# Optimization experiments

Hardware: AMD Instinct MI355X
Metric: run time of the kernel (lower is better)

## Reference

```python
import jax, jax.numpy as jnp
import numpy as np

N_NODES = 100_000
N_EDGES = 1_600_000
N_GRAPHS = 64
N_OPS = 120
OP_EMB = 32
NODE_FEAT = 140
CFG_FEAT = 18
LIN_OUT = 128
H = 64
EPS = 1e-12  # F.normalize eps


def _glorot(k, shape):
    s = (6.0 / (shape[0] + shape[1])) ** 0.5
    return jax.random.uniform(k, shape, jnp.float32, -s, s)


def setup_inputs() -> dict:
    key = jax.random.key(0)
    ks = iter(jax.random.split(key, 40))
    inp = {
        "node_feat": jax.random.normal(next(ks), (N_NODES, NODE_FEAT), jnp.float32),
        "node_config_feat": jax.random.normal(next(ks), (N_NODES, CFG_FEAT), jnp.float32),
        "node_opcode": jax.random.randint(next(ks), (N_NODES,), 0, N_OPS, jnp.int32),
        "edge_index": jax.random.randint(next(ks), (2, N_EDGES), 0, N_NODES, jnp.int32),
        # contiguous graph assignment -> every one of the 64 graphs is non-empty
        "batch": ((jnp.arange(N_NODES) * N_GRAPHS) // N_NODES).astype(jnp.int32),
        "op_emb": jax.random.normal(next(ks), (N_OPS, OP_EMB), jnp.float32),
        "lin_w": _glorot(next(ks), (NODE_FEAT + OP_EMB + CFG_FEAT, LIN_OUT)),
        "lin_b": jnp.zeros((LIN_OUT,), jnp.float32),
        "post_w": _glorot(next(ks), (H, 1)),
        "post_b": jnp.zeros((1,), jnp.float32),
    }
    in_dims = [LIN_OUT, H, H]
    for l, d in enumerate(in_dims):
        inp[f"proj_w{l}"] = _glorot(next(ks), (d, d))
        inp[f"proj_b{l}"] = jnp.zeros((d,), jnp.float32)
        inp[f"wl{l}"] = _glorot(next(ks), (d, H))
        inp[f"bl{l}"] = jnp.zeros((H,), jnp.float32)
        inp[f"wr{l}"] = _glorot(next(ks), (d, H))
    return inp


def _sage_conv(x, src, dst, pw, pb, wl, bl, wr):
    # PyG SAGEConv(normalize=True, project=True): messages use projected x,
    # root term uses the un-projected x; mean aggregation over in-edges.
    xp = jax.nn.relu(x @ pw + pb)                                  # (N, d)
    msg = jax.ops.segment_sum(xp[src], dst, num_segments=N_NODES)  # (N, d)
    deg = jax.ops.segment_sum(jnp.ones((src.shape[0],), x.dtype), dst,
                              num_segments=N_NODES)
    mean = msg / jnp.maximum(deg, 1.0)[:, None]
    out = mean @ wl + bl + x @ wr                                   # (N, H)
    n = jnp.linalg.norm(out, axis=-1, keepdims=True)
    return out / jnp.maximum(n, EPS)


def reference(node_feat, node_config_feat, node_opcode, edge_index, batch,
              op_emb, lin_w, lin_b, post_w, post_b,
              proj_w0, proj_b0, wl0, bl0, wr0,
              proj_w1, proj_b1, wl1, bl1, wr1,
              proj_w2, proj_b2, wl2, bl2, wr2):
    x = jnp.concatenate([node_feat, op_emb[node_opcode], node_config_feat], axis=-1)
    x = jax.nn.relu(x @ lin_w + lin_b)  # (N, 128)
    src, dst = edge_index[0], edge_index[1]
    layers = [(proj_w0, proj_b0, wl0, bl0, wr0),
              (proj_w1, proj_b1, wl1, bl1, wr1),
              (proj_w2, proj_b2, wl2, bl2, wr2)]
    for pw, pb, wl, bl, wr in layers:
        x = _sage_conv(x, src, dst, pw, pb, wl, bl, wr)
    # global max pool + global mean pool per graph
    x_max = jax.ops.segment_max(x, batch, num_segments=N_GRAPHS)
    cnt = jax.ops.segment_sum(jnp.ones((x.shape[0],), x.dtype), batch,
                              num_segments=N_GRAPHS)
    x_mean = jax.ops.segment_sum(x, batch, num_segments=N_GRAPHS) / cnt[:, None]
    x_graph = x_max + x_mean
    x_graph = x_graph / jnp.linalg.norm(x_graph, axis=-1, keepdims=True)
    return x_graph @ post_w + post_b  # (B, 1)
```

## Files before the change

### kernel.cpp

```cpp
#include <hip/hip_runtime.h>
#include <hip/hip_bf16.h>
#include <math.h>

#define N_NODES   100000
#define N_EDGES   1600000
#define N_GRAPHS  64
#define NF_D      140
#define OP_EMB_D  32
#define CFG_D     18
#define K_EMB     192
#define NB_SCAN   391

typedef __attribute__((ext_vector_type(8))) short short8;
typedef __attribute__((ext_vector_type(4))) float f32x4;

__device__ __forceinline__ unsigned fenc(float f) {
    unsigned u = __float_as_uint(f);
    return (u & 0x80000000u) ? ~u : (u | 0x80000000u);
}
__device__ __forceinline__ float fdec(unsigned u) {
    unsigned v = (u & 0x80000000u) ? (u & 0x7FFFFFFFu) : ~u;
    return __uint_as_float(v);
}
__device__ __forceinline__ unsigned short f2bf(float f) {
    unsigned u = __float_as_uint(f);
    return (unsigned short)((u + 0x7FFFu + ((u >> 16) & 1u)) >> 16);
}
__device__ __forceinline__ float bf2f(unsigned short h) {
    return __uint_as_float((unsigned)h << 16);
}
__device__ __forceinline__ short8 ld_frag(const unsigned short* p) {
    union { uint4 u; short8 s; } c;
    c.u = *(const uint4*)p;
    return c.s;
}


__global__ void hist_kernel(const int* __restrict__ dst, int* __restrict__ cnt) {
    int e = blockIdx.x * blockDim.x + threadIdx.x;
    if (e < N_EDGES) atomicAdd(&cnt[__builtin_nontemporal_load(dst + e)], 1);
}

__global__ __launch_bounds__(256) void blocksum_kernel(const int* __restrict__ cnt,
                                                       int* __restrict__ bsum) {
    const int tid = threadIdx.x, lane = tid & 63, wave = tid >> 6;
    int i = blockIdx.x * 256 + tid;
    int v = (i < N_NODES) ? cnt[i] : 0;
    #pragma unroll
    for (int off = 32; off > 0; off >>= 1) v += __shfl_xor(v, off, 64);
    __shared__ int wsum[4];
    if (lane == 0) wsum[wave] = v;
    __syncthreads();
    if (tid == 0) bsum[blockIdx.x] = wsum[0] + wsum[1] + wsum[2] + wsum[3];
}

__global__ __launch_bounds__(512) void scanbsum_kernel(int* __restrict__ bsum) {
    __shared__ int s[512];
    const int t = threadIdx.x;
    int v0 = (t < NB_SCAN) ? bsum[t] : 0;
    s[t] = v0;
    __syncthreads();
    for (int off = 1; off < 512; off <<= 1) {
        int add = (t >= off) ? s[t - off] : 0;
        __syncthreads();
        s[t] += add;
        __syncthreads();
    }
    if (t < NB_SCAN) bsum[t] = s[t] - v0;
}

__global__ __launch_bounds__(256) void offsets_kernel(int* __restrict__ cnt,
                                                      const int* __restrict__ bsum,
                                                      int* __restrict__ row_start) {
    const int t = threadIdx.x;
    const int i = blockIdx.x * 256 + t;
    int v0 = (i < N_NODES) ? cnt[i] : 0;
    __shared__ int s[256];
    s[t] = v0;
    __syncthreads();
    for (int off = 1; off < 256; off <<= 1) {
        int add = (t >= off) ? s[t - off] : 0;
        __syncthreads();
        s[t] += add;
        __syncthreads();
    }
    const int excl = s[t] - v0 + bsum[blockIdx.x];
    if (i < N_NODES) {
        row_start[i] = excl;
        cnt[i] = excl;
    }
    if (i == N_NODES - 1) row_start[N_NODES] = excl + v0;
}

__global__ void fill_kernel(const int* __restrict__ src, const int* __restrict__ dst,
                            int* __restrict__ cursor, int* __restrict__ nbr) {
    const int range = blockIdx.x & 7;
    const int lo = range * (N_NODES / 8);
    const int hi = lo + (N_NODES / 8);
    const int groups = gridDim.x >> 3;
    const int sub = blockIdx.x >> 3;
    for (int e = sub * blockDim.x + threadIdx.x; e < N_EDGES;
         e += groups * blockDim.x) {
        const int d = __builtin_nontemporal_load(dst + e);
        if (d >= lo && d < hi) {
            const int s = __builtin_nontemporal_load(src + e);
            const int slot = atomicAdd(&cursor[d], 1);
            nbr[slot] = s;
        }
    }
}


__global__ __launch_bounds__(256) void concat_kernel(
    const float* __restrict__ node_feat, const float* __restrict__ cfg,
    const int* __restrict__ opcode, const float* __restrict__ op_emb,
    unsigned short* __restrict__ x0)
{
    const long long total = (long long)N_NODES * 96;
    for (long long idx = (long long)blockIdx.x * blockDim.x + threadIdx.x;
         idx < total; idx += (long long)gridDim.x * blockDim.x) {
        const int n  = (int)(idx / 96);
        const int c  = 2 * (int)(idx % 96);
        float2 v;
        if (c < NF_D) {
            v = *(const float2*)(node_feat + (long long)n * NF_D + c);
        } else if (c < NF_D + OP_EMB_D) {
            const int op = opcode[n];
            v = *(const float2*)(op_emb + op * OP_EMB_D + (c - NF_D));
        } else if (c < 190) {
            v = *(const float2*)(cfg + (long long)n * CFG_D + (c - NF_D - OP_EMB_D));
        } else {
            v.x = 0.f; v.y = 0.f;
        }
        const unsigned pk = ((unsigned)f2bf(v.y) << 16) | (unsigned)f2bf(v.x);
        *(unsigned*)(x0 + (long long)n * K_EMB + c) = pk;
    }
}

struct WDesc { const float* src; unsigned short* dst; int K, Ksrc, M, off; };
struct WPack { WDesc d[10]; int total; };

__global__ __launch_bounds__(256) void pack_w_kernel(WPack p) {
    const int idx = blockIdx.x * blockDim.x + threadIdx.x;
    if (idx >= p.total) return;
    #pragma unroll
    for (int i = 0; i < 10; ++i) {
        const WDesc d = p.d[i];
        if (idx >= d.off && idx < d.off + d.K * d.M) {
            const int r    = idx - d.off;
            const int kc   = r / (d.M * 32);
            const int rem  = r % (d.M * 32);
            const int mt   = rem / 512;
            const int rem2 = rem % 512;
            const int lane = rem2 >> 3;
            const int j    = rem2 & 7;
            const int k = kc * 32 + (lane >> 4) * 8 + j;
            const int m = mt * 16 + (lane & 15);
            const float v = (k < d.Ksrc) ? d.src[(long long)k * d.M + m] : 0.f;
            d.dst[r] = f2bf(v);
            return;
        }
    }
}

template <int M, int K, bool BIAS, bool RELU, bool OBF16>
__global__ __launch_bounds__(256) void mfma_gemm(
    const unsigned short* __restrict__ x,
    const unsigned short* __restrict__ wpk, const float* __restrict__ b,
    void* __restrict__ outv, int N)
{
    constexpr int MT = M / 16;
    constexpr int KC = K / 32;
    const int tid = threadIdx.x, wave = tid >> 6, lane = tid & 63;
    const int wid = blockIdx.x * 4 + wave;
    if (wid >= (N >> 5)) return;
    const int nb   = wid << 5;
    const int l15  = lane & 15;
    const int quad = lane >> 4;

    f32x4 acc[2][MT];
    #pragma unroll
    for (int mt = 0; mt < MT; ++mt) {
        #pragma unroll
        for (int r = 0; r < 4; ++r) {
            const float bv = BIAS ? b[mt * 16 + quad * 4 + r] : 0.f;
            acc[0][mt][r] = bv;
            acc[1][mt][r] = bv;
        }
    }
    #pragma unroll
    for (int kc = 0; kc < KC; ++kc) {
        const short8 b0 = ld_frag(x + (long long)(nb + l15)      * K + kc * 32 + quad * 8);
        const short8 b1 = ld_frag(x + (long long)(nb + 16 + l15) * K + kc * 32 + quad * 8);
        #pragma unroll
        for (int mt = 0; mt < MT; ++mt) {
            const short8 a = ld_frag(wpk + ((long long)(kc * MT + mt) * 64 + lane) * 8);
            acc[0][mt] = __builtin_amdgcn_mfma_f32_16x16x32_bf16(a, b0, acc[0][mt], 0, 0, 0);
            acc[1][mt] = __builtin_amdgcn_mfma_f32_16x16x32_bf16(a, b1, acc[1][mt], 0, 0, 0);
        }
    }
    #pragma unroll
    for (int s = 0; s < 2; ++s) {
        const long long row = nb + s * 16 + l15;
        if (OBF16) {
            unsigned short* orow = (unsigned short*)outv + row * M;
            #pragma unroll
            for (int mt = 0; mt < MT; ++mt) {
                float f0 = acc[s][mt][0], f1 = acc[s][mt][1];
                float f2 = acc[s][mt][2], f3 = acc[s][mt][3];
                if (RELU) {
                    f0 = fmaxf(f0, 0.f); f1 = fmaxf(f1, 0.f);
                    f2 = fmaxf(f2, 0.f); f3 = fmaxf(f3, 0.f);
                }
                uint2 pk;
                pk.x = ((unsigned)f2bf(f1) << 16) | (unsigned)f2bf(f0);
                pk.y = ((unsigned)f2bf(f3) << 16) | (unsigned)f2bf(f2);
                *(uint2*)(orow + mt * 16 + quad * 4) = pk;
            }
        } else {
            float* orow = (float*)outv + row * M;
            #pragma unroll
            for (int mt = 0; mt < MT; ++mt) {
                f32x4 v = acc[s][mt];
                if (RELU) {
                    v[0] = fmaxf(v[0], 0.f); v[1] = fmaxf(v[1], 0.f);
                    v[2] = fmaxf(v[2], 0.f); v[3] = fmaxf(v[3], 0.f);
                }
                *(f32x4*)(orow + mt * 16 + quad * 4) = v;
            }
        }
    }
}

template <bool OBF16>
__global__ __launch_bounds__(256, 8) void combine_kernel(
    const int* __restrict__ row_start, const int* __restrict__ nbr,
    const unsigned short* __restrict__ yp, const float* __restrict__ r,
    void* __restrict__ out)
{
    const int tid = threadIdx.x, wave = tid >> 6, lane = tid & 63;
    for (int n = blockIdx.x * 4 + wave; n < N_NODES; n += gridDim.x * 4) {
        const int rs = row_start[n], re = row_start[n + 1];
        float macc[8];
        #pragma unroll
        for (int q = 0; q < 8; ++q) macc[q] = 0.f;
        for (int eb = rs; eb < re; eb += 64) {
            const int cnt = min(64, re - eb);
            const int my = (eb + lane < re) ? nbr[eb + lane] : 0;
            for (int j2 = 0; j2 < cnt; j2 += 8) {
                #pragma unroll
                for (int q = 0; q < 8; ++q) {
                    const int jj = j2 + q;
                    const int s = __shfl(my, (jj < cnt) ? jj : 0, 64);
                    const float v = bf2f(yp[(long long)s * 64 + lane]);
                    if (jj < cnt) macc[q] += v;
                }
            }
        }
        const float m = ((macc[0] + macc[1]) + (macc[2] + macc[3]))
                      + ((macc[4] + macc[5]) + (macc[6] + macc[7]));
        float acc = r[(long long)n * 64 + lane] + m / fmaxf((float)(re - rs), 1.0f);
        float sq = acc * acc;
        #pragma unroll
        for (int off = 32; off > 0; off >>= 1) sq += __shfl_xor(sq, off, 64);
        const float res = acc / fmaxf(sqrtf(sq), 1e-12f);
        if (OBF16)
            ((unsigned short*)out)[(long long)n * 64 + lane] = f2bf(res);
        else
            ((float*)out)[(long long)n * 64 + lane] = res;
    }
}


__global__ __launch_bounds__(256) void pool_kernel(
    const float* __restrict__ x, const int* __restrict__ batch,
    float* __restrict__ gsum, unsigned* __restrict__ gmax, float* __restrict__ gcnt)
{
    __shared__ float    lsum[2][64];
    __shared__ unsigned lmax[2][64];
    __shared__ int      lcnt[2];
    const int tid = threadIdx.x, wave = tid >> 6, lane = tid & 63;
    if (tid < 128) { lsum[tid >> 6][tid & 63] = 0.f; lmax[tid >> 6][tid & 63] = 0u; }
    if (tid < 2) lcnt[tid] = 0;
    __syncthreads();
    const int base = blockIdx.x * 256;
    const int g0 = batch[base];
    float a0 = 0.f, a1 = 0.f, x0 = -INFINITY, x1 = -INFINITY;
    int c0 = 0, c1 = 0;
    for (int nn = 0; nn < 64; ++nn) {
        const int n = base + wave * 64 + nn;
        if (n >= N_NODES) break;
        const float v = x[(long long)n * 64 + lane];
        const int slot = batch[n] - g0;
        if (slot == 0)      { a0 += v; x0 = fmaxf(x0, v); c0++; }
        else if (slot == 1) { a1 += v; x1 = fmaxf(x1, v); c1++; }
        else {
            const int g = g0 + slot;
            atomicAdd(&gsum[g * 64 + lane], v);
            atomicMax(&gmax[g * 64 + lane], fenc(v));
            if (lane == 0) atomicAdd(&gcnt[g], 1.f);
        }
    }
    if (c0) { atomicAdd(&lsum[0][lane], a0); atomicMax(&lmax[0][lane], fenc(x0));
              if (lane == 0) atomicAdd(&lcnt[0], c0); }
    if (c1) { atomicAdd(&lsum[1][lane], a1); atomicMax(&lmax[1][lane], fenc(x1));
              if (lane == 0) atomicAdd(&lcnt[1], c1); }
    __syncthreads();
    if (tid < 128) {
        const int slot = tid >> 6, k = tid & 63;
        if (lcnt[slot] > 0) {
            const int g = g0 + slot;
            atomicAdd(&gsum[g * 64 + k], lsum[slot][k]);
            atomicMax(&gmax[g * 64 + k], lmax[slot][k]);
            if (k == 0) atomicAdd(&gcnt[g], (float)lcnt[slot]);
        }
    }
}

__global__ void finalize_kernel(const float* __restrict__ gsum, const unsigned* __restrict__ gmax,
                                const float* __restrict__ gcnt, const float* __restrict__ post_w,
                                const float* __restrict__ post_b, float* __restrict__ out)
{
    const int g = blockIdx.x;
    const int k = threadIdx.x;
    const float cnt = gcnt[g];
    const float v = fdec(gmax[g * 64 + k]) + gsum[g * 64 + k] / cnt;
    const float w = post_w[k];
    float sq = v * v, dw = v * w;
    #pragma unroll
    for (int off = 32; off > 0; off >>= 1) {
        sq += __shfl_xor(sq, off, 64);
        dw += __shfl_xor(dw, off, 64);
    }
    if (k == 0) out[g] = dw / sqrtf(sq) + post_b[0];
}

extern "C" void kernel_launch(void* const* d_in, const int* in_sizes, int n_in,
                              void* d_out, int out_size, void* d_ws, size_t ws_size,
                              hipStream_t stream)
{
    const float* node_feat = (const float*)d_in[0];
    const float* cfg       = (const float*)d_in[1];
    const int*   opcode    = (const int*)  d_in[2];
    const int*   edge      = (const int*)  d_in[3];
    const int*   batch     = (const int*)  d_in[4];
    const float* op_emb    = (const float*)d_in[5];
    const float* lin_w     = (const float*)d_in[6];
    const float* lin_b     = (const float*)d_in[7];
    const float* post_w    = (const float*)d_in[8];
    const float* post_b    = (const float*)d_in[9];
    const float* pw[3] = {(const float*)d_in[10], (const float*)d_in[15], (const float*)d_in[20]};
    const float* pb[3] = {(const float*)d_in[11], (const float*)d_in[16], (const float*)d_in[21]};
    const float* wl[3] = {(const float*)d_in[12], (const float*)d_in[17], (const float*)d_in[22]};
    const float* bl[3] = {(const float*)d_in[13], (const float*)d_in[18], (const float*)d_in[23]};
    const float* wr[3] = {(const float*)d_in[14], (const float*)d_in[19], (const float*)d_in[24]};
    const int* srcp = edge;
    const int* dstp = edge + N_EDGES;

    float* ws   = (float*)d_ws;
    int*   nbr       = (int*)(ws + 32000000);
    int*   row_start = (int*)(ws + 33600000);
    int*   cnt       = (int*)(ws + 33700064);
    int*   bsum      = (int*)(ws + 33800064);
    float* gsum      = ws + 33825152;
    float* gcnt      = ws + 33829248;
    unsigned* gmax   = (unsigned*)(ws + 33829312);
    unsigned short* wpk_base = (unsigned short*)(ws + 34000000);

    const int OFF_EMB = 0;
    const int OFF_PW0 = 24576;
    const int OFF_WL0 = 24576 + 16384;
    const int OFF_WR0 = OFF_WL0 + 8192;
    const int OFF_PW1 = OFF_WR0 + 8192;
    const int OFF_WL1 = OFF_PW1 + 4096;
    const int OFF_WR1 = OFF_WL1 + 4096;
    const int OFF_PW2 = OFF_WR1 + 4096;
    const int OFF_WL2 = OFF_PW2 + 4096;
    const int OFF_WR2 = OFF_WL2 + 4096;
    const int W_TOTAL = OFF_WR2 + 4096;

    unsigned short* A_bf    = (unsigned short*)ws;
    unsigned short* C2_bf   = (unsigned short*)ws;
    float*          C3      = ws;
    unsigned short* C1_bf   = (unsigned short*)(ws + 6400000);
    unsigned short* X0_bf   = (unsigned short*)(ws + 12800000);
    unsigned short* xp128_bf= (unsigned short*)(ws + 12800000);
    unsigned short* xp64_bf = (unsigned short*)(ws + 12800000);
    float*          r       = ws + 19200000;
    unsigned short* yp      = (unsigned short*)(ws + 25600000);

    hipMemsetAsync(cnt, 0, (size_t)N_NODES * 4, stream);
    hipMemsetAsync(gsum, 0, (size_t)(4096 + 64 + 4096) * 4, stream);

    WPack wp;
    wp.d[0] = { lin_w, wpk_base + OFF_EMB, K_EMB, 190, 128, OFF_EMB };
    wp.d[1] = { pw[0], wpk_base + OFF_PW0, 128, 128, 128, OFF_PW0 };
    wp.d[2] = { wl[0], wpk_base + OFF_WL0, 128, 128,  64, OFF_WL0 };
    wp.d[3] = { wr[0], wpk_base + OFF_WR0, 128, 128,  64, OFF_WR0 };
    wp.d[4] = { pw[1], wpk_base + OFF_PW1,  64,  64,  64, OFF_PW1 };
    wp.d[5] = { wl[1], wpk_base + OFF_WL1,  64,  64,  64, OFF_WL1 };
    wp.d[6] = { wr[1], wpk_base + OFF_WR1,  64,  64,  64, OFF_WR1 };
    wp.d[7] = { pw[2], wpk_base + OFF_PW2,  64,  64,  64, OFF_PW2 };
    wp.d[8] = { wl[2], wpk_base + OFF_WL2,  64,  64,  64, OFF_WL2 };
    wp.d[9] = { wr[2], wpk_base + OFF_WR2,  64,  64,  64, OFF_WR2 };
    wp.total = W_TOTAL;
    pack_w_kernel<<<(W_TOTAL + 255) / 256, 256, 0, stream>>>(wp);

    hist_kernel<<<(N_EDGES + 255) / 256, 256, 0, stream>>>(dstp, cnt);
    blocksum_kernel<<<NB_SCAN, 256, 0, stream>>>(cnt, bsum);
    scanbsum_kernel<<<1, 512, 0, stream>>>(bsum);
    offsets_kernel<<<NB_SCAN, 256, 0, stream>>>(cnt, bsum, row_start);
    fill_kernel<<<8 * 256, 256, 0, stream>>>(srcp, dstp, cnt, nbr);

    concat_kernel<<<4096, 256, 0, stream>>>(node_feat, cfg, opcode, op_emb, X0_bf);

    const int GW = (N_NODES / 32 + 3) / 4;

    mfma_gemm<128, 192, true, true, true><<<GW, 256, 0, stream>>>(
        X0_bf, wpk_base + OFF_EMB, lin_b, A_bf, N_NODES);

    mfma_gemm<128, 128, true,  true,  true ><<<GW, 256, 0, stream>>>(
        A_bf, wpk_base + OFF_PW0, pb[0], xp128_bf, N_NODES);
    mfma_gemm< 64, 128, false, false, true ><<<GW, 256, 0, stream>>>(
        xp128_bf, wpk_base + OFF_WL0, nullptr, yp, N_NODES);
    mfma_gemm< 64, 128, true,  false, false><<<GW, 256, 0, stream>>>(
        A_bf, wpk_base + OFF_WR0, bl[0], r, N_NODES);
    combine_kernel<true><<<2048, 256, 0, stream>>>(row_start, nbr, yp, r, C1_bf);

    mfma_gemm< 64, 64, true,  true,  true ><<<GW, 256, 0, stream>>>(
        C1_bf, wpk_base + OFF_PW1, pb[1], xp64_bf, N_NODES);
    mfma_gemm< 64, 64, false, false, true ><<<GW, 256, 0, stream>>>(
        xp64_bf, wpk_base + OFF_WL1, nullptr, yp, N_NODES);
    mfma_gemm< 64, 64, true,  false, false><<<GW, 256, 0, stream>>>(
        C1_bf, wpk_base + OFF_WR1, bl[1], r, N_NODES);
    combine_kernel<true><<<2048, 256, 0, stream>>>(row_start, nbr, yp, r, C2_bf);

    mfma_gemm< 64, 64, true,  true,  true ><<<GW, 256, 0, stream>>>(
        C2_bf, wpk_base + OFF_PW2, pb[2], xp64_bf, N_NODES);
    mfma_gemm< 64, 64, false, false, true ><<<GW, 256, 0, stream>>>(
        xp64_bf, wpk_base + OFF_WL2, nullptr, yp, N_NODES);
    mfma_gemm< 64, 64, true,  false, false><<<GW, 256, 0, stream>>>(
        C2_bf, wpk_base + OFF_WR2, bl[2], r, N_NODES);
    combine_kernel<false><<<2048, 256, 0, stream>>>(row_start, nbr, yp, r, C3);

    pool_kernel<<<NB_SCAN, 256, 0, stream>>>(C3, batch, gsum, gmax, gcnt);
    finalize_kernel<<<N_GRAPHS, 64, 0, stream>>>(gsum, gmax, gcnt, post_w, post_b,
                                                 (float*)d_out);
}
```

Baseline: 661.7 us.

## Fuse per-layer projection, neighbor and root GEMMs into one kernel

Each SAGE layer used three separate GEMM launches: projection with ReLU written to global memory, a second GEMM reading it back for the neighbor weights, and a root GEMM re-reading the input. A new fused kernel reads the input tile once, computes the projection and root outputs together, stages the ReLU'd bf16 projection in per-wave shared memory, and applies the neighbor weights from there. This removes the xp intermediate round trip through global memory and two launches per layer, at the cost of more accumulator registers and shared memory per block, which may lower occupancy.

```diff
diff --git a/kernel.cpp b/kernel.cpp
--- a/kernel.cpp
+++ b/kernel.cpp
@@ -232,6 +232,113 @@
     }
 }
 
+template <int D>
+__global__ __launch_bounds__(256) void fused_layer(
+    const unsigned short* __restrict__ x,
+    const unsigned short* __restrict__ wpw, const float* __restrict__ pb,
+    const unsigned short* __restrict__ wwl,
+    const unsigned short* __restrict__ wwr, const float* __restrict__ bl,
+    unsigned short* __restrict__ yp, float* __restrict__ rout, int N)
+{
+    constexpr int MT  = D / 16;
+    constexpr int KC  = D / 32;
+    constexpr int LST = D + 8;
+    __shared__ unsigned short xpl[4][32][LST];
+    const int tid = threadIdx.x, wave = tid >> 6, lane = tid & 63;
+    const int wid = blockIdx.x * 4 + wave;
+    if (wid >= (N >> 5)) return;
+    const int nb   = wid << 5;
+    const int l15  = lane & 15;
+    const int quad = lane >> 4;
+
+    f32x4 axp[2][MT];
+    f32x4 ar[2][4];
+    #pragma unroll
+    for (int mt = 0; mt < MT; ++mt) {
+        #pragma unroll
+        for (int q = 0; q < 4; ++q) {
+            const float bv = pb[mt * 16 + quad * 4 + q];
+            axp[0][mt][q] = bv;
+            axp[1][mt][q] = bv;
+        }
+    }
+    #pragma unroll
+    for (int mt = 0; mt < 4; ++mt) {
+        #pragma unroll
+        for (int q = 0; q < 4; ++q) {
+            const float bv = bl[mt * 16 + quad * 4 + q];
+            ar[0][mt][q] = bv;
+            ar[1][mt][q] = bv;
+        }
+    }
+    #pragma unroll
+    for (int kc = 0; kc < KC; ++kc) {
+        const short8 b0 = ld_frag(x + (long long)(nb + l15)      * D + kc * 32 + quad * 8);
+        const short8 b1 = ld_frag(x + (long long)(nb + 16 + l15) * D + kc * 32 + quad * 8);
+        #pragma unroll
+        for (int mt = 0; mt < MT; ++mt) {
+            const short8 a = ld_frag(wpw + ((long long)(kc * MT + mt) * 64 + lane) * 8);
+            axp[0][mt] = __builtin_amdgcn_mfma_f32_16x16x32_bf16(a, b0, axp[0][mt], 0, 0, 0);
+            axp[1][mt] = __builtin_amdgcn_mfma_f32_16x16x32_bf16(a, b1, axp[1][mt], 0, 0, 0);
+        }
+        #pragma unroll
+        for (int mt = 0; mt < 4; ++mt) {
+            const short8 a = ld_frag(wwr + ((long long)(kc * 4 + mt) * 64 + lane) * 8);
+            ar[0][mt] = __builtin_amdgcn_mfma_f32_16x16x32_bf16(a, b0, ar[0][mt], 0, 0, 0);
+            ar[1][mt] = __builtin_amdgcn_mfma_f32_16x16x32_bf16(a, b1, ar[1][mt], 0, 0, 0);
+        }
+    }
+    #pragma unroll
+    for (int s = 0; s < 2; ++s) {
+        float* orow = rout + (long long)(nb + s * 16 + l15) * 64;
+        #pragma unroll
+        for (int mt = 0; mt < 4; ++mt)
+            *(f32x4*)(orow + mt * 16 + quad * 4) = ar[s][mt];
+    }
+    #pragma unroll
+    for (int s = 0; s < 2; ++s) {
+        #pragma unroll
+        for (int mt = 0; mt < MT; ++mt) {
+            float f0 = fmaxf(axp[s][mt][0], 0.f), f1 = fmaxf(axp[s][mt][1], 0.f);
+            float f2 = fmaxf(axp[s][mt][2], 0.f), f3 = fmaxf(axp[s][mt][3], 0.f);
+            uint2 pk;
+            pk.x = ((unsigned)f2bf(f1) << 16) | (unsigned)f2bf(f0);
+            pk.y = ((unsigned)f2bf(f3) << 16) | (unsigned)f2bf(f2);
+            *(uint2*)&xpl[wave][s * 16 + l15][mt * 16 + quad * 4] = pk;
+        }
+    }
+    asm volatile("s_waitcnt lgkmcnt(0)" ::: "memory");
+
+    f32x4 ay[2][4];
+    #pragma unroll
+    for (int mt = 0; mt < 4; ++mt) {
+        #pragma unroll
+        for (int q = 0; q < 4; ++q) { ay[0][mt][q] = 0.f; ay[1][mt][q] = 0.f; }
+    }
+    #pragma unroll
+    for (int kc = 0; kc < KC; ++kc) {
+        const short8 b0 = ld_frag(&xpl[wave][l15]     [kc * 32 + quad * 8]);
+        const short8 b1 = ld_frag(&xpl[wave][16 + l15][kc * 32 + quad * 8]);
+        #pragma unroll
+        for (int mt = 0; mt < 4; ++mt) {
+            const short8 a = ld_frag(wwl + ((long long)(kc * 4 + mt) * 64 + lane) * 8);
+            ay[0][mt] = __builtin_amdgcn_mfma_f32_16x16x32_bf16(a, b0, ay[0][mt], 0, 0, 0);
+            ay[1][mt] = __builtin_amdgcn_mfma_f32_16x16x32_bf16(a, b1, ay[1][mt], 0, 0, 0);
+        }
+    }
+    #pragma unroll
+    for (int s = 0; s < 2; ++s) {
+        unsigned short* orow = yp + (long long)(nb + s * 16 + l15) * 64;
+        #pragma unroll
+        for (int mt = 0; mt < 4; ++mt) {
+            uint2 pk;
+            pk.x = ((unsigned)f2bf(ay[s][mt][1]) << 16) | (unsigned)f2bf(ay[s][mt][0]);
+            pk.y = ((unsigned)f2bf(ay[s][mt][3]) << 16) | (unsigned)f2bf(ay[s][mt][2]);
+            *(uint2*)(orow + mt * 16 + quad * 4) = pk;
+        }
+    }
+}
+
 template <bool OBF16>
 __global__ __launch_bounds__(256, 8) void combine_kernel(
     const int* __restrict__ row_start, const int* __restrict__ nbr,
@@ -384,8 +491,6 @@
     float*          C3      = ws;
     unsigned short* C1_bf   = (unsigned short*)(ws + 6400000);
     unsigned short* X0_bf   = (unsigned short*)(ws + 12800000);
-    unsigned short* xp128_bf= (unsigned short*)(ws + 12800000);
-    unsigned short* xp64_bf = (unsigned short*)(ws + 12800000);
     float*          r       = ws + 19200000;
     unsigned short* yp      = (unsigned short*)(ws + 25600000);
 
@@ -419,28 +524,19 @@
     mfma_gemm<128, 192, true, true, true><<<GW, 256, 0, stream>>>(
         X0_bf, wpk_base + OFF_EMB, lin_b, A_bf, N_NODES);
 
-    mfma_gemm<128, 128, true,  true,  true ><<<GW, 256, 0, stream>>>(
-        A_bf, wpk_base + OFF_PW0, pb[0], xp128_bf, N_NODES);
-    mfma_gemm< 64, 128, false, false, true ><<<GW, 256, 0, stream>>>(
-        xp128_bf, wpk_base + OFF_WL0, nullptr, yp, N_NODES);
-    mfma_gemm< 64, 128, true,  false, false><<<GW, 256, 0, stream>>>(
-        A_bf, wpk_base + OFF_WR0, bl[0], r, N_NODES);
+    fused_layer<128><<<GW, 256, 0, stream>>>(
+        A_bf, wpk_base + OFF_PW0, pb[0], wpk_base + OFF_WL0,
+        wpk_base + OFF_WR0, bl[0], yp, r, N_NODES);
     combine_kernel<true><<<2048, 256, 0, stream>>>(row_start, nbr, yp, r, C1_bf);
 
-    mfma_gemm< 64, 64, true,  true,  true ><<<GW, 256, 0, stream>>>(
-        C1_bf, wpk_base + OFF_PW1, pb[1], xp64_bf, N_NODES);
-    mfma_gemm< 64, 64, false, false, true ><<<GW, 256, 0, stream>>>(
-        xp64_bf, wpk_base + OFF_WL1, nullptr, yp, N_NODES);
-    mfma_gemm< 64, 64, true,  false, false><<<GW, 256, 0, stream>>>(
-        C1_bf, wpk_base + OFF_WR1, bl[1], r, N_NODES);
+    fused_layer<64><<<GW, 256, 0, stream>>>(
+        C1_bf, wpk_base + OFF_PW1, pb[1], wpk_base + OFF_WL1,
+        wpk_base + OFF_WR1, bl[1], yp, r, N_NODES);
     combine_kernel<true><<<2048, 256, 0, stream>>>(row_start, nbr, yp, r, C2_bf);
 
-    mfma_gemm< 64, 64, true,  true,  true ><<<GW, 256, 0, stream>>>(
-        C2_bf, wpk_base + OFF_PW2, pb[2], xp64_bf, N_NODES);
-    mfma_gemm< 64, 64, false, false, true ><<<GW, 256, 0, stream>>>(
-        xp64_bf, wpk_base + OFF_WL2, nullptr, yp, N_NODES);
-    mfma_gemm< 64, 64, true,  false, false><<<GW, 256, 0, stream>>>(
-        C2_bf, wpk_base + OFF_WR2, bl[2], r, N_NODES);
+    fused_layer<64><<<GW, 256, 0, stream>>>(
+        C2_bf, wpk_base + OFF_PW2, pb[2], wpk_base + OFF_WL2,
+        wpk_base + OFF_WR2, bl[2], yp, r, N_NODES);
     combine_kernel<false><<<2048, 256, 0, stream>>>(row_start, nbr, yp, r, C3);
 
     pool_kernel<<<NB_SCAN, 256, 0, stream>>>(C3, batch, gsum, gmax, gcnt);
```

New measurement: 629.8 us. 1.05x faster.
